# Kernel optimization log

Hardware: AMD Instinct MI355X
Metric: run time of the kernel (lower is better)

Reference implementation:

```python
import jax, jax.numpy as jnp
import numpy as np

NUM_HEADS = 16
ROPE_BASE = 10000.0

def _rope(x):
    # x: (B, T, H, hd), rotate-half 1D RoPE over temporal axis
    B, T, H, hd = x.shape
    inv_freq = 1.0 / (ROPE_BASE ** (jnp.arange(0, hd, 2, dtype=jnp.float32) / hd))  # (hd/2,)
    freqs = jnp.arange(T, dtype=jnp.float32)[:, None] * inv_freq[None, :]            # (T, hd/2)
    emb = jnp.concatenate([freqs, freqs], axis=-1)                                    # (T, hd)
    cos = jnp.cos(emb)[None, :, None, :]
    sin = jnp.sin(emb)[None, :, None, :]
    x1, x2 = jnp.split(x, 2, axis=-1)
    rot = jnp.concatenate([-x2, x1], axis=-1)
    return x * cos + rot * sin

def setup_inputs() -> dict:
    key = jax.random.key(0)
    ks = jax.random.split(key, 7)
    B, T, S, D = 4, 16, 256, 2048
    std = 0.02
    return {
        'v_p': jax.random.normal(ks[0], (B, T, S, D), jnp.float32),
        'v_f': jax.random.normal(ks[1], (B, T, S, D), jnp.float32),
        'a_p': jax.random.normal(ks[2], (B, T, D), jnp.float32),
        'a_f': jax.random.normal(ks[3], (B, T, D), jnp.float32),
        'W_qkv': jax.random.normal(ks[4], (D, 3 * D), jnp.float32) * std,
        'W_proj': jax.random.normal(ks[5], (D, D), jnp.float32) * std,
        'b_proj': jnp.zeros((D,), jnp.float32),
    }

def reference(v_p, v_f, a_p, a_f, W_qkv, W_proj, b_proj):
    B, T_p, S, D = v_p.shape
    T_f = v_f.shape[1]
    H = NUM_HEADS
    hd = D // H
    scale = hd ** -0.5
    # pool spatial dim and concatenate streams: [v_p, v_f, a_p, a_f]
    tokens = jnp.concatenate([v_p.mean(axis=2), v_f.mean(axis=2), a_p, a_f], axis=1)  # (B, T, D)
    T = tokens.shape[1]
    qkv = tokens @ W_qkv  # qkv_bias=False
    q, k, v = jnp.split(qkv, 3, axis=-1)
    q = q.reshape(B, T, H, hd)
    k = k.reshape(B, T, H, hd)
    v = v.reshape(B, T, H, hd)
    q = _rope(q)
    k = _rope(k)
    scores = jnp.einsum('bqhd,bkhd->bhqk', q, k) * scale
    causal_mask = jnp.triu(jnp.ones((T, T), dtype=bool), k=1)
    scores = jnp.where(causal_mask[None, None], -jnp.inf, scores)
    attn = jax.nn.softmax(scores, axis=-1)
    out = jnp.einsum('bhqk,bkhd->bqhd', attn, v).reshape(B, T, D)
    out = out @ W_proj + b_proj
    v_p_out = jnp.broadcast_to(out[:, :T_p, None, :], (B, T_p, S, D))
    v_f_out = jnp.broadcast_to(out[:, T_p:T_p + T_f, None, :], (B, T_f, S, D))
    a_p_out = out[:, T_p + T_f:T_p + T_f + T_p]
    a_f_out = out[:, T_p + T_f + T_p:]
    return (v_p_out, v_f_out, a_p_out, a_f_out)
```

## Files before the change

### kernel.cpp

```cpp
#include <hip/hip_runtime.h>
#include <hip/hip_bf16.h>
#include <stdint.h>


using bf16x8v = __attribute__((ext_vector_type(8))) __bf16;
using f32x4v  = __attribute__((ext_vector_type(4))) float;

union Pack8 { __bf16 h[8]; uint4 u; };

__device__ __forceinline__ int swz(int r, int c) {
    return (r << 6) + ((c ^ (r & 7)) << 3);
}

__global__ __launch_bounds__(256) void prep_w_kernel(
    const float* __restrict__ W_qkv, const float* __restrict__ W_proj,
    __bf16* __restrict__ Wt_qkv, __bf16* __restrict__ Wt_proj)
{
    int bid = blockIdx.x;
    const float* src; __bf16* dst; int N, tile;
    if (bid < 3072) { src = W_qkv;  dst = Wt_qkv;  N = 6144; tile = bid; }
    else            { src = W_proj; dst = Wt_proj; N = 2048; tile = bid - 3072; }
    __shared__ float Ls[64][68];
    int tiles_n = N >> 6;
    int tn = tile % tiles_n;
    int tk = tile / tiles_n;
    int t = threadIdx.x;
    int rb = t >> 4;
    int c4 = (t & 15) << 2;
    #pragma unroll
    for (int s = 0; s < 4; ++s) {
        int r = rb + (s << 4);
        float4 v = *reinterpret_cast<const float4*>(
            src + (size_t)(tk * 64 + r) * N + tn * 64 + c4);
        *reinterpret_cast<float4*>(&Ls[r][c4]) = v;
    }
    __syncthreads();
    int c  = t >> 2;
    int r0 = (t & 3) << 4;
    Pack8 p0, p1;
    #pragma unroll
    for (int i = 0; i < 8; ++i) p0.h[i] = (__bf16)Ls[r0 + i][c];
    #pragma unroll
    for (int i = 0; i < 8; ++i) p1.h[i] = (__bf16)Ls[r0 + 8 + i][c];
    __bf16* drow = dst + (size_t)(tn * 64 + c) * 2048 + tk * 64 + r0;
    *reinterpret_cast<uint4*>(drow)     = p0.u;
    *reinterpret_cast<uint4*>(drow + 8) = p1.u;
}

__global__ __launch_bounds__(256) void mean_stage1_kernel(
    const float* __restrict__ v_p, const float* __restrict__ v_f,
    float* __restrict__ partials)
{
    int bid = blockIdx.x;
    int which  = bid >> 10;
    int rem    = bid & 1023;
    int row    = rem >> 4;
    int dchunk = (rem >> 3) & 1;
    int schunk = rem & 7;
    int d = (dchunk << 10) + (threadIdx.x << 2);
    const float* src = (which ? v_f : v_p) + ((size_t)row << 19)
                     + ((size_t)(schunk << 5) << 11) + d;
    float4 a = {0.f, 0.f, 0.f, 0.f};
    #pragma unroll 8
    for (int s = 0; s < 32; ++s) {
        float4 x = *reinterpret_cast<const float4*>(src + ((size_t)s << 11));
        a.x += x.x; a.y += x.y; a.z += x.z; a.w += x.w;
    }
    int pr = which * 64 + row;
    *reinterpret_cast<float4*>(&partials[(size_t)((pr << 3) + schunk) * 2048 + d]) = a;
}

__global__ __launch_bounds__(256) void tokens_finish_kernel(
    const float* __restrict__ partials, const float* __restrict__ a_p,
    const float* __restrict__ a_f, __bf16* __restrict__ tokens_bf)
{
    int bid = blockIdx.x;
    if (bid < 128) {
        int idx = (bid * 256 + threadIdx.x) * 8;
        int r = idx >> 11;
        int d = idx & 2047;
        float s[8];
        #pragma unroll
        for (int i = 0; i < 8; ++i) s[i] = 0.f;
        #pragma unroll
        for (int sc = 0; sc < 8; ++sc) {
            const float* p = partials + (size_t)((r << 3) + sc) * 2048 + d;
            float4 x0 = *reinterpret_cast<const float4*>(p);
            float4 x1 = *reinterpret_cast<const float4*>(p + 4);
            s[0] += x0.x; s[1] += x0.y; s[2] += x0.z; s[3] += x0.w;
            s[4] += x1.x; s[5] += x1.y; s[6] += x1.z; s[7] += x1.w;
        }
        const float inv = 1.f / 256.f;
        int which = r >> 6, rr = r & 63;
        int b = rr >> 4, tt = rr & 15;
        int tokrow = b * 64 + which * 16 + tt;
        Pack8 p;
        #pragma unroll
        for (int i = 0; i < 8; ++i) p.h[i] = (__bf16)(s[i] * inv);
        *reinterpret_cast<uint4*>(&tokens_bf[(size_t)tokrow * 2048 + d]) = p.u;
    } else {
        int g = (bid - 128) * 256 + threadIdx.x;
        int which = g >> 14;
        int j = g & 16383;
        int b = j >> 12;
        int rr = j & 4095;
        int tt = rr >> 8;
        int gq = rr & 255;
        const float* src = (which ? a_f : a_p) + (size_t)(b * 16 + tt) * 2048 + gq * 8;
        float4 x0 = *reinterpret_cast<const float4*>(src);
        float4 x1 = *reinterpret_cast<const float4*>(src + 4);
        Pack8 p;
        p.h[0] = (__bf16)x0.x; p.h[1] = (__bf16)x0.y; p.h[2] = (__bf16)x0.z; p.h[3] = (__bf16)x0.w;
        p.h[4] = (__bf16)x1.x; p.h[5] = (__bf16)x1.y; p.h[6] = (__bf16)x1.z; p.h[7] = (__bf16)x1.w;
        int tokrow = b * 64 + 32 + which * 16 + tt;
        *reinterpret_cast<uint4*>(&tokens_bf[(size_t)tokrow * 2048 + gq * 8]) = p.u;
    }
}

__global__ __launch_bounds__(256) void gemm_bf16_kernel(
    const __bf16* __restrict__ A, const __bf16* __restrict__ Bt,
    const float* __restrict__ bias, float* __restrict__ C, int N)
{
    __shared__ __bf16 As[4096];
    __shared__ __bf16 Bs[4096];
    const int t = threadIdx.x;
    const int m0 = blockIdx.y << 6;
    const int n0 = blockIdx.x << 6;
    const int lane = t & 63;
    const int wm = (t >> 6) << 4;
    const int lrow = lane & 15;
    const int lk = lane >> 4;
    const int srow = t >> 3;
    const int sc = t & 7;
    const __bf16* gA = A  + (size_t)(m0 + srow) * 2048 + (sc << 3);
    const __bf16* gB = Bt + (size_t)(n0 + srow) * 2048 + (sc << 3);
    const int wA0 = swz(srow, sc), wA1 = swz(srow + 32, sc);

    f32x4v acc[4] = {{0.f,0.f,0.f,0.f},{0.f,0.f,0.f,0.f},
                     {0.f,0.f,0.f,0.f},{0.f,0.f,0.f,0.f}};
    uint4 pa0, pa1, pb0, pb1;
    pa0 = *reinterpret_cast<const uint4*>(gA);
    pa1 = *reinterpret_cast<const uint4*>(gA + 32 * 2048);
    pb0 = *reinterpret_cast<const uint4*>(gB);
    pb1 = *reinterpret_cast<const uint4*>(gB + 32 * 2048);

    for (int kt = 0; kt < 32; ++kt) {
        __syncthreads();
        *reinterpret_cast<uint4*>(&As[wA0]) = pa0;
        *reinterpret_cast<uint4*>(&As[wA1]) = pa1;
        *reinterpret_cast<uint4*>(&Bs[wA0]) = pb0;
        *reinterpret_cast<uint4*>(&Bs[wA1]) = pb1;
        __syncthreads();
        if (kt < 31) {
            const __bf16* nA = gA + (kt + 1) * 64;
            const __bf16* nB = gB + (kt + 1) * 64;
            pa0 = *reinterpret_cast<const uint4*>(nA);
            pa1 = *reinterpret_cast<const uint4*>(nA + 32 * 2048);
            pb0 = *reinterpret_cast<const uint4*>(nB);
            pb1 = *reinterpret_cast<const uint4*>(nB + 32 * 2048);
        }
        #pragma unroll
        for (int s = 0; s < 2; ++s) {
            int cA = (s << 2) + lk;
            bf16x8v af = *reinterpret_cast<const bf16x8v*>(&As[swz(wm + lrow, cA)]);
            #pragma unroll
            for (int j = 0; j < 4; ++j) {
                bf16x8v bf = *reinterpret_cast<const bf16x8v*>(&Bs[swz((j << 4) + lrow, cA)]);
                acc[j] = __builtin_amdgcn_mfma_f32_16x16x32_bf16(af, bf, acc[j], 0, 0, 0);
            }
        }
    }
    #pragma unroll
    for (int j = 0; j < 4; ++j) {
        int col = n0 + (j << 4) + lrow;
        float bv = bias ? bias[col] : 0.f;
        #pragma unroll
        for (int e = 0; e < 4; ++e) {
            int row = m0 + wm + (lk << 2) + e;
            C[(size_t)row * N + col] = acc[j][e] + bv;
        }
    }
}

__global__ __launch_bounds__(256) void rope_kernel(float* __restrict__ qkv)
{
    int row = blockIdx.x;
    int t = row & 63;
    float* q = qkv + (size_t)row * 6144;
    for (int i = threadIdx.x; i < 1024; i += 256) {
        int h = i >> 6;
        int d = i & 63;
        float invf = powf(10000.f, -(float)d * (1.f / 64.f));
        float ang = (float)t * invf;
        float c = cosf(ang), s = sinf(ang);
        int i0 = h * 128 + d;
        float q1 = q[i0], q2 = q[i0 + 64];
        q[i0]      = q1 * c - q2 * s;
        q[i0 + 64] = q2 * c + q1 * s;
        float* k = q + 2048;
        float k1 = k[i0], k2 = k[i0 + 64];
        k[i0]      = k1 * c - k2 * s;
        k[i0 + 64] = k2 * c + k1 * s;
    }
}

__global__ __launch_bounds__(256) void attn_kernel(
    const float* __restrict__ qkv, __bf16* __restrict__ attn_out)
{
    __shared__ float q_s[64 * 128];
    __shared__ float k_s[64 * 128];
    int b = blockIdx.x >> 4;
    int h = blockIdx.x & 15;
    int tid = threadIdx.x;
    const float* base = qkv + (size_t)(b * 64) * 6144 + h * 128;
    #pragma unroll
    for (int r = 0; r < 8; ++r) {
        int idx = tid + (r << 8);
        int t = idx >> 5;
        int d = (idx & 31) << 2;
        const float* src = base + (size_t)t * 6144 + d;
        *reinterpret_cast<float4*>(&q_s[t * 128 + d]) = *reinterpret_cast<const float4*>(src);
        *reinterpret_cast<float4*>(&k_s[t * 128 + d]) = *reinterpret_cast<const float4*>(src + 2048);
    }
    __syncthreads();
    int qi = tid >> 2;
    int g  = tid & 3;
    float pv[16];
    #pragma unroll
    for (int j = 0; j < 16; ++j) pv[j] = 0.f;
    for (int d = 0; d < 128; d += 4) {
        float4 a = *reinterpret_cast<const float4*>(&q_s[qi * 128 + d]);
        #pragma unroll
        for (int j = 0; j < 16; ++j) {
            int ki = (j << 2) + g;
            float4 bb = *reinterpret_cast<const float4*>(&k_s[ki * 128 + d]);
            pv[j] += a.x * bb.x + a.y * bb.y + a.z * bb.z + a.w * bb.w;
        }
    }
    const float scale = 0.0883883476483184405f;
    float m = -1e30f;
    #pragma unroll
    for (int j = 0; j < 16; ++j) {
        int ki = (j << 2) + g;
        pv[j] = (ki <= qi) ? pv[j] * scale : -1e30f;
        m = fmaxf(m, pv[j]);
    }
    m = fmaxf(m, __shfl_xor(m, 1));
    m = fmaxf(m, __shfl_xor(m, 2));
    float l = 0.f;
    #pragma unroll
    for (int j = 0; j < 16; ++j) {
        float e = (pv[j] > -1e29f) ? expf(pv[j] - m) : 0.f;
        pv[j] = e;
        l += e;
    }
    l += __shfl_xor(l, 1);
    l += __shfl_xor(l, 2);
    float inv_l = 1.f / l;
    __syncthreads();
    float* p_s = q_s;
    #pragma unroll
    for (int j = 0; j < 16; ++j) p_s[qi * 65 + (j << 2) + g] = pv[j] * inv_l;
    float* v_s = k_s;
    #pragma unroll
    for (int r = 0; r < 8; ++r) {
        int idx = tid + (r << 8);
        int t = idx >> 5;
        int d = (idx & 31) << 2;
        *reinterpret_cast<float4*>(&v_s[t * 128 + d]) =
            *reinterpret_cast<const float4*>(base + (size_t)t * 6144 + 4096 + d);
    }
    __syncthreads();
    int d0 = g << 5;
    float4 acc[8];
    #pragma unroll
    for (int u = 0; u < 8; ++u) acc[u] = {0.f, 0.f, 0.f, 0.f};
    for (int ki = 0; ki < 64; ++ki) {
        float p = p_s[qi * 65 + ki];
        #pragma unroll
        for (int u = 0; u < 8; ++u) {
            float4 vv = *reinterpret_cast<const float4*>(&v_s[ki * 128 + d0 + (u << 2)]);
            acc[u].x += p * vv.x;
            acc[u].y += p * vv.y;
            acc[u].z += p * vv.z;
            acc[u].w += p * vv.w;
        }
    }
    __bf16* orow = attn_out + (size_t)(b * 64 + qi) * 2048 + h * 128 + d0;
    #pragma unroll
    for (int v = 0; v < 4; ++v) {
        Pack8 p;
        float4 a0 = acc[2 * v], a1 = acc[2 * v + 1];
        p.h[0] = (__bf16)a0.x; p.h[1] = (__bf16)a0.y; p.h[2] = (__bf16)a0.z; p.h[3] = (__bf16)a0.w;
        p.h[4] = (__bf16)a1.x; p.h[5] = (__bf16)a1.y; p.h[6] = (__bf16)a1.z; p.h[7] = (__bf16)a1.w;
        *reinterpret_cast<uint4*>(orow + v * 8) = p.u;
    }
}

__global__ __launch_bounds__(256) void outputs_kernel(
    const float* __restrict__ outp, float* __restrict__ d_out)
{
    int bid = blockIdx.x;
    if (bid < 2048) {
        int which = bid >> 10;
        int rem = bid & 1023;
        int row = rem >> 4;
        int schunk = rem & 15;
        int b = row >> 4;
        int t = row & 15;
        const float* src = outp + (size_t)(b * 64 + (which << 4) + t) * 2048 + threadIdx.x * 8;
        float4 o0 = *reinterpret_cast<const float4*>(src);
        float4 o1 = *reinterpret_cast<const float4*>(src + 4);
        size_t base = (size_t)which * 33554432 +
                      ((size_t)row * 256 + (size_t)schunk * 16) * 2048 + threadIdx.x * 8;
        float* dst = d_out + base;
        #pragma unroll
        for (int s = 0; s < 16; ++s) {
            *reinterpret_cast<float4*>(dst + (size_t)s * 2048)     = o0;
            *reinterpret_cast<float4*>(dst + (size_t)s * 2048 + 4) = o1;
        }
    } else {
        int g = (bid - 2048) * 256 + threadIdx.x;
        int which = g >> 14;
        int j = g & 16383;
        int b = j >> 12;
        int rr = j & 4095;
        int tt = rr >> 8;
        int gq = rr & 255;
        const float* src = outp + (size_t)(b * 64 + 32 + (which << 4) + tt) * 2048 + gq * 8;
        float4 x0 = *reinterpret_cast<const float4*>(src);
        float4 x1 = *reinterpret_cast<const float4*>(src + 4);
        float* dst = d_out + 67108864 + (size_t)which * 131072 +
                     (size_t)(b * 16 + tt) * 2048 + gq * 8;
        *reinterpret_cast<float4*>(dst)     = x0;
        *reinterpret_cast<float4*>(dst + 4) = x1;
    }
}

extern "C" void kernel_launch(void* const* d_in, const int* in_sizes, int n_in,
                              void* d_out, int out_size, void* d_ws, size_t ws_size,
                              hipStream_t stream)
{
    const float* v_p    = (const float*)d_in[0];
    const float* v_f    = (const float*)d_in[1];
    const float* a_p    = (const float*)d_in[2];
    const float* a_f    = (const float*)d_in[3];
    const float* W_qkv  = (const float*)d_in[4];
    const float* W_proj = (const float*)d_in[5];
    const float* b_proj = (const float*)d_in[6];
    float* out_f = (float*)d_out;

    char* ws = (char*)d_ws;
    __bf16* tokens_bf = (__bf16*)(ws);
    __bf16* Wt_qkv    = (__bf16*)(ws + 1048576);
    __bf16* Wt_proj   = (__bf16*)(ws + 26214400);
    float*  qkv       = (float*)(ws + 34603008);
    __bf16* attn_bf   = (__bf16*)(ws + 40894464);
    float*  outp      = (float*)(ws + 41943040);
    float*  partials  = (float*)(ws + 44040192);

    prep_w_kernel<<<4096, 256, 0, stream>>>(W_qkv, W_proj, Wt_qkv, Wt_proj);
    mean_stage1_kernel<<<2048, 256, 0, stream>>>(v_p, v_f, partials);
    tokens_finish_kernel<<<256, 256, 0, stream>>>(partials, a_p, a_f, tokens_bf);
    gemm_bf16_kernel<<<dim3(96, 4), 256, 0, stream>>>(tokens_bf, Wt_qkv, nullptr, qkv, 6144);
    rope_kernel<<<256, 256, 0, stream>>>(qkv);
    attn_kernel<<<64, 256, 0, stream>>>(qkv, attn_bf);
    gemm_bf16_kernel<<<dim3(32, 4), 256, 0, stream>>>(attn_bf, Wt_proj, b_proj, outp, 2048);
    outputs_kernel<<<2176, 256, 0, stream>>>(outp, out_f);
}
```

Measured before the change: 241.1 us.

## Fuse RoPE into attention load and use direct global-to-LDS GEMM loads

The separate RoPE kernel is removed and the rotation is applied while the attention kernel loads q and k into shared memory, computing inverse frequencies with exp2f. This saves one kernel launch and a read-modify-write pass over q and k. The GEMM now uses global_load_lds to copy tiles straight into swizzled LDS, replacing the register-staged loads. That removes the register prefetch, so each tile's global load is no longer overlapped with the previous tile's MFMA work.

```diff
diff --git a/kernel.cpp b/kernel.cpp
--- a/kernel.cpp
+++ b/kernel.cpp
@@ -127,38 +127,43 @@
     const int m0 = blockIdx.y << 6;
     const int n0 = blockIdx.x << 6;
     const int lane = t & 63;
-    const int wm = (t >> 6) << 4;
+    const int w = t >> 6;
+    const int wm = w << 4;
     const int lrow = lane & 15;
     const int lk = lane >> 4;
-    const int srow = t >> 3;
-    const int sc = t & 7;
-    const __bf16* gA = A  + (size_t)(m0 + srow) * 2048 + (sc << 3);
-    const __bf16* gB = Bt + (size_t)(n0 + srow) * 2048 + (sc << 3);
-    const int wA0 = swz(srow, sc), wA1 = swz(srow + 32, sc);
+    const int srl = lane >> 3;
+    const int schunk = lane & 7;
 
     f32x4v acc[4] = {{0.f,0.f,0.f,0.f},{0.f,0.f,0.f,0.f},
                      {0.f,0.f,0.f,0.f},{0.f,0.f,0.f,0.f}};
-    uint4 pa0, pa1, pb0, pb1;
-    pa0 = *reinterpret_cast<const uint4*>(gA);
-    pa1 = *reinterpret_cast<const uint4*>(gA + 32 * 2048);
-    pb0 = *reinterpret_cast<const uint4*>(gB);
-    pb1 = *reinterpret_cast<const uint4*>(gB + 32 * 2048);
+
+    int row_c0 = (w << 4) + srl;
+    int row_c1 = row_c0 + 8;
+    const __bf16* gA0 = A  + (size_t)(m0 + row_c0) * 2048 + ((schunk ^ (row_c0 & 7)) << 3);
+    const __bf16* gA1 = A  + (size_t)(m0 + row_c1) * 2048 + ((schunk ^ (row_c1 & 7)) << 3);
+    const __bf16* gB0 = Bt + (size_t)(n0 + row_c0) * 2048 + ((schunk ^ (row_c0 & 7)) << 3);
+    const __bf16* gB1 = Bt + (size_t)(n0 + row_c1) * 2048 + ((schunk ^ (row_c1 & 7)) << 3);
+    __bf16* lA0 = &As[(w << 4) << 6];
+    __bf16* lA1 = &As[((w << 4) + 8) << 6];
+    __bf16* lB0 = &Bs[(w << 4) << 6];
+    __bf16* lB1 = &Bs[((w << 4) + 8) << 6];
 
     for (int kt = 0; kt < 32; ++kt) {
         __syncthreads();
-        *reinterpret_cast<uint4*>(&As[wA0]) = pa0;
-        *reinterpret_cast<uint4*>(&As[wA1]) = pa1;
-        *reinterpret_cast<uint4*>(&Bs[wA0]) = pb0;
-        *reinterpret_cast<uint4*>(&Bs[wA1]) = pb1;
+        int ko = kt << 6;
+        __builtin_amdgcn_global_load_lds(
+            (const __attribute__((address_space(1))) void*)(gA0 + ko),
+            (__attribute__((address_space(3))) void*)lA0, 16, 0, 0);
+        __builtin_amdgcn_global_load_lds(
+            (const __attribute__((address_space(1))) void*)(gA1 + ko),
+            (__attribute__((address_space(3))) void*)lA1, 16, 0, 0);
+        __builtin_amdgcn_global_load_lds(
+            (const __attribute__((address_space(1))) void*)(gB0 + ko),
+            (__attribute__((address_space(3))) void*)lB0, 16, 0, 0);
+        __builtin_amdgcn_global_load_lds(
+            (const __attribute__((address_space(1))) void*)(gB1 + ko),
+            (__attribute__((address_space(3))) void*)lB1, 16, 0, 0);
         __syncthreads();
-        if (kt < 31) {
-            const __bf16* nA = gA + (kt + 1) * 64;
-            const __bf16* nB = gB + (kt + 1) * 64;
-            pa0 = *reinterpret_cast<const uint4*>(nA);
-            pa1 = *reinterpret_cast<const uint4*>(nA + 32 * 2048);
-            pb0 = *reinterpret_cast<const uint4*>(nB);
-            pb1 = *reinterpret_cast<const uint4*>(nB + 32 * 2048);
-        }
         #pragma unroll
         for (int s = 0; s < 2; ++s) {
             int cA = (s << 2) + lk;
@@ -182,28 +187,6 @@
     }
 }
 
-__global__ __launch_bounds__(256) void rope_kernel(float* __restrict__ qkv)
-{
-    int row = blockIdx.x;
-    int t = row & 63;
-    float* q = qkv + (size_t)row * 6144;
-    for (int i = threadIdx.x; i < 1024; i += 256) {
-        int h = i >> 6;
-        int d = i & 63;
-        float invf = powf(10000.f, -(float)d * (1.f / 64.f));
-        float ang = (float)t * invf;
-        float c = cosf(ang), s = sinf(ang);
-        int i0 = h * 128 + d;
-        float q1 = q[i0], q2 = q[i0 + 64];
-        q[i0]      = q1 * c - q2 * s;
-        q[i0 + 64] = q2 * c + q1 * s;
-        float* k = q + 2048;
-        float k1 = k[i0], k2 = k[i0 + 64];
-        k[i0]      = k1 * c - k2 * s;
-        k[i0 + 64] = k2 * c + k1 * s;
-    }
-}
-
 __global__ __launch_bounds__(256) void attn_kernel(
     const float* __restrict__ qkv, __bf16* __restrict__ attn_out)
 {
@@ -213,14 +196,39 @@
     int h = blockIdx.x & 15;
     int tid = threadIdx.x;
     const float* base = qkv + (size_t)(b * 64) * 6144 + h * 128;
-    #pragma unroll
-    for (int r = 0; r < 8; ++r) {
+    const float L2 = 0.20762050593046012f;
+    #pragma unroll
+    for (int r = 0; r < 4; ++r) {
         int idx = tid + (r << 8);
-        int t = idx >> 5;
-        int d = (idx & 31) << 2;
-        const float* src = base + (size_t)t * 6144 + d;
-        *reinterpret_cast<float4*>(&q_s[t * 128 + d]) = *reinterpret_cast<const float4*>(src);
-        *reinterpret_cast<float4*>(&k_s[t * 128 + d]) = *reinterpret_cast<const float4*>(src + 2048);
+        int tq = idx >> 4;
+        int d = (idx & 15) << 2;
+        const float* srcr = base + (size_t)tq * 6144;
+        float4 q1 = *reinterpret_cast<const float4*>(srcr + d);
+        float4 q2 = *reinterpret_cast<const float4*>(srcr + d + 64);
+        float4 k1 = *reinterpret_cast<const float4*>(srcr + 2048 + d);
+        float4 k2 = *reinterpret_cast<const float4*>(srcr + 2048 + d + 64);
+        float ft = (float)tq;
+        float a0 = ft * exp2f(-(float)(d + 0) * L2);
+        float a1 = ft * exp2f(-(float)(d + 1) * L2);
+        float a2 = ft * exp2f(-(float)(d + 2) * L2);
+        float a3 = ft * exp2f(-(float)(d + 3) * L2);
+        float c0 = cosf(a0), s0 = sinf(a0);
+        float c1 = cosf(a1), s1 = sinf(a1);
+        float c2 = cosf(a2), s2 = sinf(a2);
+        float c3 = cosf(a3), s3 = sinf(a3);
+        float4 qa, qb, ka, kb;
+        qa.x = q1.x * c0 - q2.x * s0;  qb.x = q2.x * c0 + q1.x * s0;
+        qa.y = q1.y * c1 - q2.y * s1;  qb.y = q2.y * c1 + q1.y * s1;
+        qa.z = q1.z * c2 - q2.z * s2;  qb.z = q2.z * c2 + q1.z * s2;
+        qa.w = q1.w * c3 - q2.w * s3;  qb.w = q2.w * c3 + q1.w * s3;
+        ka.x = k1.x * c0 - k2.x * s0;  kb.x = k2.x * c0 + k1.x * s0;
+        ka.y = k1.y * c1 - k2.y * s1;  kb.y = k2.y * c1 + k1.y * s1;
+        ka.z = k1.z * c2 - k2.z * s2;  kb.z = k2.z * c2 + k1.z * s2;
+        ka.w = k1.w * c3 - k2.w * s3;  kb.w = k2.w * c3 + k1.w * s3;
+        *reinterpret_cast<float4*>(&q_s[tq * 128 + d])      = qa;
+        *reinterpret_cast<float4*>(&q_s[tq * 128 + d + 64]) = qb;
+        *reinterpret_cast<float4*>(&k_s[tq * 128 + d])      = ka;
+        *reinterpret_cast<float4*>(&k_s[tq * 128 + d + 64]) = kb;
     }
     __syncthreads();
     int qi = tid >> 2;
@@ -363,7 +371,6 @@
     mean_stage1_kernel<<<2048, 256, 0, stream>>>(v_p, v_f, partials);
     tokens_finish_kernel<<<256, 256, 0, stream>>>(partials, a_p, a_f, tokens_bf);
     gemm_bf16_kernel<<<dim3(96, 4), 256, 0, stream>>>(tokens_bf, Wt_qkv, nullptr, qkv, 6144);
-    rope_kernel<<<256, 256, 0, stream>>>(qkv);
     attn_kernel<<<64, 256, 0, stream>>>(qkv, attn_bf);
     gemm_bf16_kernel<<<dim3(32, 4), 256, 0, stream>>>(attn_bf, Wt_proj, b_proj, outp, 2048);
     outputs_kernel<<<2176, 256, 0, stream>>>(outp, out_f);
```

Measured after the change: 241.1 us. Within noise of the previous version (+0.0%).
